# Optimization experiments

Measured on AMD Instinct MI355X. Metric: run time of the kernel, lower is better.

Reference implementation:

```python
import jax, jax.numpy as jnp
import numpy as np

B, S, E = 2048, 23, 768
RED, H, NUM_LABELS = 256, 8, 25
DH = RED // H
DELTA = 0.1
EPS_LN = 1e-5


def setup_inputs() -> dict:
    key = jax.random.key(0)
    ks = jax.random.split(key, 20)
    g = lambda k, shape, fan: jax.random.normal(k, shape, dtype=jnp.float32) * (1.0 / np.sqrt(fan))
    inp = {
        'cls_embeddings': jax.random.normal(ks[0], (B, S, E), dtype=jnp.float32),
        'existing_mask': jax.random.randint(ks[1], (B, S), 0, 2, dtype=jnp.int32),
        'missing_emb': g(ks[2], (S, E), E),
        'W1': g(ks[3], (E // 2, E), E), 'b1': jnp.zeros((E // 2,), jnp.float32),
        'W2': g(ks[4], (RED, E // 2), E // 2), 'b2': jnp.zeros((RED,), jnp.float32),
        'ln_g': jnp.ones((RED,), jnp.float32), 'ln_b': jnp.zeros((RED,), jnp.float32),
        'Wq': g(ks[5], (RED, RED), RED), 'bq': jnp.zeros((RED,), jnp.float32),
        'Wk': g(ks[6], (RED, RED), RED), 'bk': jnp.zeros((RED,), jnp.float32),
        'Wv': g(ks[7], (RED, RED), RED), 'bv': jnp.zeros((RED,), jnp.float32),
        'Wo': g(ks[8], (RED, RED), RED), 'bo': jnp.zeros((RED,), jnp.float32),
        'Wp': g(ks[9], (NUM_LABELS, RED), RED), 'bp': jnp.zeros((NUM_LABELS,), jnp.float32),
    }
    return inp


def _layer_norm(x, g, b):
    mu = jnp.mean(x, axis=-1, keepdims=True)
    var = jnp.mean(jnp.square(x - mu), axis=-1, keepdims=True)
    return (x - mu) * jax.lax.rsqrt(var + EPS_LN) * g + b


def _forward(cls_embeddings, existing_mask, missing_emb, W1, b1, W2, b2, ln_g, ln_b,
             Wq, bq, Wk, bk, Wv, bv, Wo, bo, Wp, bp):
    exist = existing_mask > 0                              # [B,S] bool
    # Gather: existing sections use BERT CLS, missing slots use learned embeddings
    sec = jnp.where(exist[..., None], cls_embeddings, missing_emb[None])  # [B,S,E]
    # SectionDimReducer (exact-erf GELU as in nn.GELU default)
    h = jax.nn.gelu(sec @ W1.T + b1, approximate=False)
    h = jax.nn.gelu(h @ W2.T + b2, approximate=False)
    red = _layer_norm(h, ln_g, ln_b)                       # [B,S,RED]
    # Tiny MHA: every slot queries the existing sections of its own EHR
    q = (red @ Wq.T + bq).reshape(B, S, H, DH)
    k = (red @ Wk.T + bk).reshape(B, S, H, DH)
    v = (red @ Wv.T + bv).reshape(B, S, H, DH)
    scores = jnp.einsum('bqhd,bkhd->bhqk', q, k) / np.sqrt(DH)
    scores = jnp.where(exist[:, None, None, :], scores, -1e9)
    attn = jax.nn.softmax(scores, axis=-1)                 # [B,H,S,S]
    ctx = jnp.einsum('bhqk,bkhd->bqhd', attn, v).reshape(B, S, RED)
    mha_out = ctx @ Wo.T + bo                              # [B,S,RED]
    # Scatter: only missing slots (of EHRs with >=1 existing section) are replaced
    any_exist = jnp.any(exist, axis=1)                     # [B]
    use_attn = (~exist) & any_exist[:, None]               # [B,S]
    updated = jnp.where(use_attn[..., None], mha_out, red)
    # margin-based orthogonality loss on section embeddings
    norm = updated / jnp.maximum(jnp.linalg.norm(updated, axis=-1, keepdims=True), 1e-8)
    gram = jnp.einsum('bid,bjd->bij', norm, norm)          # [B,S,S]
    off = 1.0 - jnp.eye(S, dtype=updated.dtype)
    loss_orth = jnp.sum(jax.nn.relu(jnp.abs(gram) - DELTA) * off) / (B * S * (S - 1))
    logits = updated.mean(axis=1) @ Wp.T + bp              # [B,NUM_LABELS]
    return loss_orth, logits


def reference(cls_embeddings, existing_mask, missing_emb, W1, b1, W2, b2, ln_g, ln_b,
              Wq, bq, Wk, bk, Wv, bv, Wo, bo, Wp, bp):
    return _forward(cls_embeddings, existing_mask, missing_emb, W1, b1, W2, b2, ln_g, ln_b,
                    Wq, bq, Wk, bk, Wv, bv, Wo, bo, Wp, bp)
```

## Files before the change

### kernel.cpp

```cpp
#include <hip/hip_runtime.h>

typedef unsigned short u16;
typedef unsigned int u32;
typedef __attribute__((ext_vector_type(8))) short short8;
typedef __attribute__((ext_vector_type(4))) float f32x4;

struct __align__(8) us4 { u16 x, y, z, w; };

__device__ __forceinline__ float bf1(u16 v){ return __uint_as_float(((u32)v) << 16); }
__device__ __forceinline__ float bflo(u32 u){ return __uint_as_float(u << 16); }
__device__ __forceinline__ float bfhi(u32 u){ return __uint_as_float(u & 0xFFFF0000u); }
__device__ __forceinline__ u16 fbf(float f){
    u32 u = __float_as_uint(f);
    return (u16)((u + 0x7FFFu + ((u >> 16) & 1u)) >> 16);
}
__device__ __forceinline__ float gelu_exact(float x){
    return 0.5f * x * (1.0f + erff(x * 0.70710678118654752f));
}
__device__ __forceinline__ void unp8(uint4 u, float* f){
    f[0]=bflo(u.x); f[1]=bfhi(u.x); f[2]=bflo(u.y); f[3]=bfhi(u.y);
    f[4]=bflo(u.z); f[5]=bfhi(u.z); f[6]=bflo(u.w); f[7]=bfhi(u.w);
}
__device__ __forceinline__ uint4 pack8(float4 a, float4 b){
    uint4 u;
    u.x = (u32)fbf(a.x) | ((u32)fbf(a.y) << 16);
    u.y = (u32)fbf(a.z) | ((u32)fbf(a.w) << 16);
    u.z = (u32)fbf(b.x) | ((u32)fbf(b.y) << 16);
    u.w = (u32)fbf(b.z) | ((u32)fbf(b.w) << 16);
    return u;
}

#define MFMA16(a, b, c) __builtin_amdgcn_mfma_f32_16x16x32_bf16(a, b, c, 0, 0, 0)
#define QSTR 264


__global__ __launch_bounds__(256) void wconv(
    const float* __restrict__ W1, const float* __restrict__ W2,
    const float* __restrict__ Wq, const float* __restrict__ Wk,
    const float* __restrict__ Wv, const float* __restrict__ Wo,
    const float* __restrict__ Wp, u16* __restrict__ dst)
{
    const int i = blockIdx.x * 256 + threadIdx.x;
    const float* s; int o;
    if      (i < 294912) { s = W1; o = i; }
    else if (i < 393216) { s = W2; o = i - 294912; }
    else if (i < 458752) { s = Wq; o = i - 393216; }
    else if (i < 524288) { s = Wk; o = i - 458752; }
    else if (i < 589824) { s = Wv; o = i - 524288; }
    else if (i < 655360) { s = Wo; o = i - 589824; }
    else                 { s = Wp; o = i - 655360; }
    dst[i] = fbf(s[o]);
}

__global__ __launch_bounds__(256) void gemm1_kernel(
    const float* __restrict__ cls, const int* __restrict__ mask,
    const float* __restrict__ missing, const u16* __restrict__ W,
    const float* __restrict__ bias, u16* __restrict__ C)
{
    const int K = 768, M = 384;
    __shared__ u16 As[128 * 40];
    __shared__ u16 Bs[128 * 40];
    const int tid = threadIdx.x;
    const int w = tid >> 6, lane = tid & 63;
    const int nBase = blockIdx.y * 128, mBase = blockIdx.x * 128;
    const int wr = w >> 1, wc = w & 1;
    const int r0 = tid >> 2;
    const int co = (tid & 3) * 8;
    const int frow = lane & 15, quad = lane >> 4;

    const int rowA0 = nBase + r0, rowA1 = nBase + r0 + 64;
    const float* ap0 = (mask[rowA0] > 0) ? cls + (size_t)rowA0 * 768
                                         : missing + (size_t)(rowA0 % 23) * 768;
    const float* ap1 = (mask[rowA1] > 0) ? cls + (size_t)rowA1 * 768
                                         : missing + (size_t)(rowA1 % 23) * 768;
    const u16* bp0 = W + (size_t)(mBase + r0) * K;
    const u16* bp1 = W + (size_t)(mBase + r0 + 64) * K;

    f32x4 acc[4][4];
#pragma unroll
    for (int mt = 0; mt < 4; ++mt)
#pragma unroll
        for (int nt = 0; nt < 4; ++nt) acc[mt][nt] = f32x4{0.f, 0.f, 0.f, 0.f};

    float4 a0a = *(const float4*)(ap0 + co), a0b = *(const float4*)(ap0 + co + 4);
    float4 a1a = *(const float4*)(ap1 + co), a1b = *(const float4*)(ap1 + co + 4);
    uint4 pb0 = *(const uint4*)(bp0 + co), pb1 = *(const uint4*)(bp1 + co);

    for (int k0 = 0; k0 < K; k0 += 32) {
        __syncthreads();
        *(uint4*)(As + r0 * 40 + co) = pack8(a0a, a0b);
        *(uint4*)(As + (r0 + 64) * 40 + co) = pack8(a1a, a1b);
        *(uint4*)(Bs + r0 * 40 + co) = pb0;
        *(uint4*)(Bs + (r0 + 64) * 40 + co) = pb1;
        __syncthreads();
        if (k0 + 32 < K) {
            const int kn = k0 + 32 + co;
            a0a = *(const float4*)(ap0 + kn); a0b = *(const float4*)(ap0 + kn + 4);
            a1a = *(const float4*)(ap1 + kn); a1b = *(const float4*)(ap1 + kn + 4);
            pb0 = *(const uint4*)(bp0 + kn);  pb1 = *(const uint4*)(bp1 + kn);
        }
        short8 af[4], bfv[4];
#pragma unroll
        for (int mt = 0; mt < 4; ++mt)
            af[mt] = *(const short8*)(As + (wr * 64 + mt * 16 + frow) * 40 + quad * 8);
#pragma unroll
        for (int nt = 0; nt < 4; ++nt)
            bfv[nt] = *(const short8*)(Bs + (wc * 64 + nt * 16 + frow) * 40 + quad * 8);
#pragma unroll
        for (int mt = 0; mt < 4; ++mt)
#pragma unroll
            for (int nt = 0; nt < 4; ++nt)
                acc[mt][nt] = MFMA16(af[mt], bfv[nt], acc[mt][nt]);
    }

#pragma unroll
    for (int nt = 0; nt < 4; ++nt) {
        const int col = mBase + wc * 64 + nt * 16 + frow;
        const float bv = bias[col];
#pragma unroll
        for (int mt = 0; mt < 4; ++mt)
#pragma unroll
            for (int reg = 0; reg < 4; ++reg) {
                const int row = nBase + wr * 64 + mt * 16 + quad * 4 + reg;
                C[(size_t)row * M + col] = fbf(gelu_exact(acc[mt][nt][reg] + bv));
            }
    }
}

__global__ __launch_bounds__(256) void gemm_bt(
    const u16* __restrict__ A, const u16* __restrict__ W,
    const float* __restrict__ bias, u16* __restrict__ C, int K, int M)
{
    __shared__ u16 As[128 * 40];
    __shared__ u16 Bs[128 * 40];
    const int tid = threadIdx.x;
    const int w = tid >> 6, lane = tid & 63;
    const int nBase = blockIdx.y * 128, mBase = blockIdx.x * 128;
    const int wr = w >> 1, wc = w & 1;
    const int r0 = tid >> 2;
    const int co = (tid & 3) * 8;
    const int frow = lane & 15, quad = lane >> 4;

    f32x4 acc[4][4];
#pragma unroll
    for (int mt = 0; mt < 4; ++mt)
#pragma unroll
        for (int nt = 0; nt < 4; ++nt) acc[mt][nt] = f32x4{0.f, 0.f, 0.f, 0.f};

    uint4 pa0 = *(const uint4*)(A + (size_t)(nBase + r0) * K + co);
    uint4 pa1 = *(const uint4*)(A + (size_t)(nBase + r0 + 64) * K + co);
    uint4 pb0 = *(const uint4*)(W + (size_t)(mBase + r0) * K + co);
    uint4 pb1 = *(const uint4*)(W + (size_t)(mBase + r0 + 64) * K + co);

    for (int k0 = 0; k0 < K; k0 += 32) {
        __syncthreads();
        *(uint4*)(As + r0 * 40 + co) = pa0;
        *(uint4*)(As + (r0 + 64) * 40 + co) = pa1;
        *(uint4*)(Bs + r0 * 40 + co) = pb0;
        *(uint4*)(Bs + (r0 + 64) * 40 + co) = pb1;
        __syncthreads();
        if (k0 + 32 < K) {
            const int kn = k0 + 32 + co;
            pa0 = *(const uint4*)(A + (size_t)(nBase + r0) * K + kn);
            pa1 = *(const uint4*)(A + (size_t)(nBase + r0 + 64) * K + kn);
            pb0 = *(const uint4*)(W + (size_t)(mBase + r0) * K + kn);
            pb1 = *(const uint4*)(W + (size_t)(mBase + r0 + 64) * K + kn);
        }
        short8 af[4], bfv[4];
#pragma unroll
        for (int mt = 0; mt < 4; ++mt)
            af[mt] = *(const short8*)(As + (wr * 64 + mt * 16 + frow) * 40 + quad * 8);
#pragma unroll
        for (int nt = 0; nt < 4; ++nt)
            bfv[nt] = *(const short8*)(Bs + (wc * 64 + nt * 16 + frow) * 40 + quad * 8);
#pragma unroll
        for (int mt = 0; mt < 4; ++mt)
#pragma unroll
            for (int nt = 0; nt < 4; ++nt)
                acc[mt][nt] = MFMA16(af[mt], bfv[nt], acc[mt][nt]);
    }

#pragma unroll
    for (int nt = 0; nt < 4; ++nt) {
        const int col = mBase + wc * 64 + nt * 16 + frow;
        const float bv = bias[col];
#pragma unroll
        for (int mt = 0; mt < 4; ++mt)
#pragma unroll
            for (int reg = 0; reg < 4; ++reg) {
                const int row = nBase + wr * 64 + mt * 16 + quad * 4 + reg;
                C[(size_t)row * M + col] = fbf(gelu_exact(acc[mt][nt][reg] + bv));
            }
    }
}

__device__ __forceinline__ void ln1_reg(
    const float* x, const float4& g0, const float4& g1,
    const float4& b0, const float4& b1, u16* rp)
{
    float s = x[0] + x[1] + x[2] + x[3] + x[4] + x[5] + x[6] + x[7];
    s += __shfl_xor(s, 1); s += __shfl_xor(s, 2); s += __shfl_xor(s, 4);
    s += __shfl_xor(s, 8); s += __shfl_xor(s, 16);
    const float mu = s * (1.f / 256.f);
    float v = 0.f;
#pragma unroll
    for (int e = 0; e < 8; ++e) { const float d = x[e] - mu; v += d * d; }
    v += __shfl_xor(v, 1); v += __shfl_xor(v, 2); v += __shfl_xor(v, 4);
    v += __shfl_xor(v, 8); v += __shfl_xor(v, 16);
    const float rs = rsqrtf(v * (1.f / 256.f) + 1e-5f);
    float4 ya, yb;
    ya.x = (x[0]-mu)*rs*g0.x + b0.x;
    ya.y = (x[1]-mu)*rs*g0.y + b0.y;
    ya.z = (x[2]-mu)*rs*g0.z + b0.z;
    ya.w = (x[3]-mu)*rs*g0.w + b0.w;
    yb.x = (x[4]-mu)*rs*g1.x + b1.x;
    yb.y = (x[5]-mu)*rs*g1.y + b1.y;
    yb.z = (x[6]-mu)*rs*g1.z + b1.z;
    yb.w = (x[7]-mu)*rs*g1.w + b1.w;
    *(uint4*)rp = pack8(ya, yb);
}

__device__ __forceinline__ void ln3_reg_store(
    uint4 rg0, uint4 rg1, uint4 rg2, bool has2,
    const float* __restrict__ lng, const float* __restrict__ lnb,
    u16* dstBase, int s0, int c0o)
{
    const float4 g0 = *(const float4*)(lng + c0o);
    const float4 g1 = *(const float4*)(lng + c0o + 4);
    const float4 b0 = *(const float4*)(lnb + c0o);
    const float4 b1 = *(const float4*)(lnb + c0o + 4);
    float x[8];
    unp8(rg0, x); ln1_reg(x, g0, g1, b0, b1, dstBase + s0 * QSTR + c0o);
    unp8(rg1, x); ln1_reg(x, g0, g1, b0, b1, dstBase + (s0 + 8) * QSTR + c0o);
    if (has2) { unp8(rg2, x); ln1_reg(x, g0, g1, b0, b1, dstBase + (s0 + 16) * QSTR + c0o); }
}

#define KLOOP_PF(WPTR, SRC, ACC)                                                  \
    {                                                                             \
        short8 nb0 = *(const short8*)(WPTR);                                      \
        short8 nb1 = *(const short8*)((WPTR) + 16 * 256);                         \
        short8 nb2 = *(const short8*)((WPTR) + 32 * 256);                         \
        short8 nb3 = *(const short8*)((WPTR) + 48 * 256);                         \
        for (int k0 = 0; k0 < 256; k0 += 32) {                                    \
            short8 a0 = *(const short8*)((SRC) + r0c * QSTR + k0 + quad * 8);     \
            short8 a1 = *(const short8*)((SRC) + r1c * QSTR + k0 + quad * 8);     \
            short8 c0 = nb0, c1 = nb1, c2 = nb2, c3 = nb3;                        \
            if (k0 + 32 < 256) {                                                  \
                nb0 = *(const short8*)((WPTR) + (k0 + 32));                       \
                nb1 = *(const short8*)((WPTR) + 16 * 256 + (k0 + 32));            \
                nb2 = *(const short8*)((WPTR) + 32 * 256 + (k0 + 32));            \
                nb3 = *(const short8*)((WPTR) + 48 * 256 + (k0 + 32));            \
            }                                                                     \
            ACC[0][0] = MFMA16(a0, c0, ACC[0][0]); ACC[1][0] = MFMA16(a1, c0, ACC[1][0]); \
            ACC[0][1] = MFMA16(a0, c1, ACC[0][1]); ACC[1][1] = MFMA16(a1, c1, ACC[1][1]); \
            ACC[0][2] = MFMA16(a0, c2, ACC[0][2]); ACC[1][2] = MFMA16(a1, c2, ACC[1][2]); \
            ACC[0][3] = MFMA16(a0, c3, ACC[0][3]); ACC[1][3] = MFMA16(a1, c3, ACC[1][3]); \
        }                                                                         \
    }

__global__ __launch_bounds__(256, 3) void attn_tail_kernel(
    const u16* __restrict__ redb, const int* __restrict__ mask,
    const u16* __restrict__ Wqkvb,
    const float* __restrict__ bq, const float* __restrict__ bk,
    const float* __restrict__ bv, const u16* __restrict__ Wob,
    const float* __restrict__ bo, const float* __restrict__ lng,
    const float* __restrict__ lnb, const u16* __restrict__ Wpb,
    const float* __restrict__ bp, float* __restrict__ out,
    float* __restrict__ lossAcc)
{
    __shared__ __align__(16) unsigned char SM[40960];
    u16* s_rq = (u16*)SM;
    u16* s_k  = (u16*)(SM + 12144);
    u16* s_vT = (u16*)(SM + 24288);
    int* sEx   = (int*)(SM + 40672);
    int* sMiss = (int*)(SM + 40764);
    float* sDiag = (float*)(SM + 24288);
    float* sInv  = (float*)(SM + 24384);
    float* sPool = (float*)(SM + 24480);

    const int b = blockIdx.x, t = threadIdx.x;
    const int w = t >> 6, lane = t & 63;
    const int frow = lane & 15, quad = lane >> 4;
    const int r0c = frow;
    const int r1c = (16 + frow > 22) ? 22 : 16 + frow;
    const f32x4 z4 = f32x4{0.f, 0.f, 0.f, 0.f};

    {
        const int myEx = (t < 23) ? mask[b * 23 + t] : 0;
        if (t < 23) sEx[t] = myEx;
        if (t < 64) {
            const unsigned long long ball = __ballot((t < 23) && (myEx > 0));
            if (t < 23) sMiss[t] = (ball != 0ull && myEx <= 0) ? 1 : 0;
        }
    }
    for (int i = t; i < 1024; i += 256) ((uint4*)s_vT)[i] = make_uint4(0u, 0u, 0u, 0u);

    {
        const u16* src = redb + (size_t)(b * 23) * 256;
        const int s0 = t >> 5, c0o = (t & 31) * 8;
        uint4 rg0 = *(const uint4*)(src + s0 * 256 + c0o);
        uint4 rg1 = *(const uint4*)(src + (s0 + 8) * 256 + c0o);
        uint4 rg2 = make_uint4(0u, 0u, 0u, 0u);
        const bool has2 = t < 224;
        if (has2) rg2 = *(const uint4*)(src + (s0 + 16) * 256 + c0o);
        ln3_reg_store(rg0, rg1, rg2, has2, lng, lnb, s_rq, s0, c0o);
    }
    __syncthreads();

    const int cmb = w * 64 + frow;
    {
        f32x4 ka[2][4];
#pragma unroll
        for (int mt = 0; mt < 2; ++mt)
#pragma unroll
            for (int nt = 0; nt < 4; ++nt) ka[mt][nt] = z4;
        const u16* wp = Wqkvb + (size_t)(256 + cmb) * 256 + quad * 8;
        const float bb[4] = {bk[cmb], bk[cmb + 16], bk[cmb + 32], bk[cmb + 48]};
        KLOOP_PF(wp, s_rq, ka)
#pragma unroll
        for (int nt = 0; nt < 4; ++nt) {
            const int cm = cmb + nt * 16;
#pragma unroll
            for (int mt = 0; mt < 2; ++mt)
#pragma unroll
                for (int reg = 0; reg < 4; ++reg) {
                    const int s = mt * 16 + quad * 4 + reg;
                    if (s < 23) s_k[s * QSTR + cm] = fbf(ka[mt][nt][reg] + bb[nt]);
                }
        }
    }
    {
        f32x4 va[2][4];
#pragma unroll
        for (int mt = 0; mt < 2; ++mt)
#pragma unroll
            for (int nt = 0; nt < 4; ++nt) va[mt][nt] = z4;
        const u16* wp = Wqkvb + (size_t)(512 + cmb) * 256 + quad * 8;
        const float bb[4] = {bv[cmb], bv[cmb + 16], bv[cmb + 32], bv[cmb + 48]};
        KLOOP_PF(wp, s_rq, va)
#pragma unroll
        for (int nt = 0; nt < 4; ++nt) {
            const int cm = cmb + nt * 16;
#pragma unroll
            for (int mt = 0; mt < 2; ++mt)
#pragma unroll
                for (int reg = 0; reg < 4; ++reg) {
                    const int s = mt * 16 + quad * 4 + reg;
                    if (s < 23) s_vT[cm * 32 + s] = fbf(va[mt][nt][reg] + bb[nt]);
                }
        }
    }
    {
        f32x4 qa[2][4];
#pragma unroll
        for (int mt = 0; mt < 2; ++mt)
#pragma unroll
            for (int nt = 0; nt < 4; ++nt) qa[mt][nt] = z4;
        const u16* wp = Wqkvb + (size_t)cmb * 256 + quad * 8;
        const float bb[4] = {bq[cmb], bq[cmb + 16], bq[cmb + 32], bq[cmb + 48]};
        KLOOP_PF(wp, s_rq, qa)
        __syncthreads();
#pragma unroll
        for (int nt = 0; nt < 4; ++nt) {
            const int cm = cmb + nt * 16;
#pragma unroll
            for (int mt = 0; mt < 2; ++mt)
#pragma unroll
                for (int reg = 0; reg < 4; ++reg) {
                    const int s = mt * 16 + quad * 4 + reg;
                    if (s < 23) s_rq[s * QSTR + cm] = fbf(qa[mt][nt][reg] + bb[nt]);
                }
        }
    }

    {
        const float scl = 0.17677669529663687f;
        const float m0 = (sEx[frow] > 0) ? 0.f : -1e9f;
        const float m1 = (16 + frow < 23 && sEx[16 + frow] > 0) ? 0.f : -1e9f;
#pragma unroll
        for (int hh2 = 0; hh2 < 2; ++hh2) {
            const int hb = w * 64 + hh2 * 32;
            short8 aq0 = *(const short8*)(s_rq + r0c * QSTR + hb + quad * 8);
            short8 aq1 = *(const short8*)(s_rq + r1c * QSTR + hb + quad * 8);
            short8 bk0 = *(const short8*)(s_k + r0c * QSTR + hb + quad * 8);
            short8 bk1 = *(const short8*)(s_k + r1c * QSTR + hb + quad * 8);
            f32x4 s00 = MFMA16(aq0, bk0, z4);
            f32x4 s01 = MFMA16(aq0, bk1, z4);
            f32x4 s10 = MFMA16(aq1, bk0, z4);
            f32x4 s11 = MFMA16(aq1, bk1, z4);
#pragma unroll
            for (int mt = 0; mt < 2; ++mt) {
                f32x4& c0 = mt ? s10 : s00;
                f32x4& c1 = mt ? s11 : s01;
#pragma unroll
                for (int reg = 0; reg < 4; ++reg) {
                    float v0 = c0[reg] * scl + m0;
                    float v1 = c1[reg] * scl + m1;
                    float mx = fmaxf(v0, v1);
#pragma unroll
                    for (int m = 8; m; m >>= 1) mx = fmaxf(mx, __shfl_xor(mx, m));
                    float p0 = __expf(v0 - mx), p1 = __expf(v1 - mx);
                    float sm = p0 + p1;
#pragma unroll
                    for (int m = 8; m; m >>= 1) sm += __shfl_xor(sm, m);
                    const float inv = 1.f / sm;
                    c0[reg] = p0 * inv;
                    c1[reg] = p1 * inv;
                }
            }
#pragma unroll
            for (int reg = 0; reg < 4; ++reg) {
                const int q0r = quad * 4 + reg;
                s_k[q0r * QSTR + hb + frow]      = fbf(s00[reg]);
                s_k[q0r * QSTR + hb + 16 + frow] = fbf(s01[reg]);
                const int q1r = 16 + quad * 4 + reg;
                if (q1r < 23) {
                    s_k[q1r * QSTR + hb + frow]      = fbf(s10[reg]);
                    s_k[q1r * QSTR + hb + 16 + frow] = fbf(s11[reg]);
                }
            }
            short8 pa0 = *(const short8*)(s_k + r0c * QSTR + hb + quad * 8);
            short8 pa1 = *(const short8*)(s_k + r1c * QSTR + hb + quad * 8);
            short8 bv0 = *(const short8*)(s_vT + (hb + frow) * 32 + quad * 8);
            short8 bv1 = *(const short8*)(s_vT + (hb + 16 + frow) * 32 + quad * 8);
            f32x4 c00 = MFMA16(pa0, bv0, z4);
            f32x4 c01 = MFMA16(pa0, bv1, z4);
            f32x4 c10 = MFMA16(pa1, bv0, z4);
            f32x4 c11 = MFMA16(pa1, bv1, z4);
#pragma unroll
            for (int reg = 0; reg < 4; ++reg) {
                const int q0r = quad * 4 + reg;
                s_rq[q0r * QSTR + hb + frow]      = fbf(c00[reg]);
                s_rq[q0r * QSTR + hb + 16 + frow] = fbf(c01[reg]);
                const int q1r = 16 + quad * 4 + reg;
                if (q1r < 23) {
                    s_rq[q1r * QSTR + hb + frow]      = fbf(c10[reg]);
                    s_rq[q1r * QSTR + hb + 16 + frow] = fbf(c11[reg]);
                }
            }
        }
    }
    __syncthreads();

    {
        f32x4 wacc[2][4];
#pragma unroll
        for (int mt = 0; mt < 2; ++mt)
#pragma unroll
            for (int nt = 0; nt < 4; ++nt) wacc[mt][nt] = z4;
        const u16* wp = Wob + (size_t)cmb * 256 + quad * 8;
        const float ob[4] = {bo[cmb], bo[cmb + 16], bo[cmb + 32], bo[cmb + 48]};
        KLOOP_PF(wp, s_rq, wacc)
        {
            const u16* src = redb + (size_t)(b * 23) * 256;
            const int s0 = t >> 5, c0o = (t & 31) * 8;
            uint4 rg0 = *(const uint4*)(src + s0 * 256 + c0o);
            uint4 rg1 = *(const uint4*)(src + (s0 + 8) * 256 + c0o);
            uint4 rg2 = make_uint4(0u, 0u, 0u, 0u);
            const bool has2 = t < 224;
            if (has2) rg2 = *(const uint4*)(src + (s0 + 16) * 256 + c0o);
            ln3_reg_store(rg0, rg1, rg2, has2, lng, lnb, s_k, s0, c0o);
        }
        __syncthreads();
#pragma unroll
        for (int nt = 0; nt < 4; ++nt) {
            const int col = cmb + nt * 16;
#pragma unroll
            for (int mt = 0; mt < 2; ++mt)
#pragma unroll
                for (int reg = 0; reg < 4; ++reg) {
                    const int s = mt * 16 + quad * 4 + reg;
                    if (s < 23 && sMiss[s])
                        s_k[s * QSTR + col] = fbf(wacc[mt][nt][reg] + ob[nt]);
                }
        }
    }
    __syncthreads();

    f32x4 g00 = z4, g01 = z4, g10 = z4, g11 = z4;
    if (w == 0) {
        short8 ga0 = *(const short8*)(s_k + r0c * QSTR + quad * 8);
        short8 ga1 = *(const short8*)(s_k + r1c * QSTR + quad * 8);
        for (int k0 = 0; k0 < 256; k0 += 32) {
            short8 a0 = ga0, a1 = ga1;
            if (k0 + 32 < 256) {
                ga0 = *(const short8*)(s_k + r0c * QSTR + k0 + 32 + quad * 8);
                ga1 = *(const short8*)(s_k + r1c * QSTR + k0 + 32 + quad * 8);
            }
            g00 = MFMA16(a0, a0, g00);
            g01 = MFMA16(a0, a1, g01);
            g10 = MFMA16(a1, a0, g10);
            g11 = MFMA16(a1, a1, g11);
        }
#pragma unroll
        for (int reg = 0; reg < 4; ++reg) {
            if (frow == quad * 4 + reg) {
                sDiag[frow] = g00[reg];
                if (16 + frow < 23) sDiag[16 + frow] = g11[reg];
            }
        }
    } else {
        for (int c = t - 64; c < 256; c += 192) {
            float pv = 0.f;
#pragma unroll
            for (int s = 0; s < 23; ++s) pv += bf1(s_k[s * QSTR + c]);
            sPool[c] = pv * (1.f / 23.f);
        }
    }
    __syncthreads();
    if (t < 23) sInv[t] = 1.f / fmaxf(sqrtf(sDiag[t]), 1e-8f);
    __syncthreads();

    if (w == 0) {
        float contrib = 0.f;
        const float ic0 = sInv[frow];
        const float ic1 = (16 + frow < 23) ? sInv[16 + frow] : 0.f;
        const bool c1ok = (16 + frow < 23);
#pragma unroll
        for (int reg = 0; reg < 4; ++reg) {
            const int rA = quad * 4 + reg;
            const float irA = sInv[rA];
            if (rA != frow) {
                const float cc = fabsf(g00[reg] * irA * ic0) - 0.1f;
                if (cc > 0.f) contrib += cc;
            }
            if (c1ok) {
                const float cc = fabsf(g01[reg] * irA * ic1) - 0.1f;
                if (cc > 0.f) contrib += cc;
            }
            const int rB = 16 + quad * 4 + reg;
            if (rB < 23) {
                const float irB = sInv[rB];
                {
                    const float cc = fabsf(g10[reg] * irB * ic0) - 0.1f;
                    if (cc > 0.f) contrib += cc;
                }
                if (c1ok && rB != 16 + frow) {
                    const float cc = fabsf(g11[reg] * irB * ic1) - 0.1f;
                    if (cc > 0.f) contrib += cc;
                }
            }
        }
#pragma unroll
        for (int m = 32; m; m >>= 1) contrib += __shfl_xor(contrib, m);
        if (lane == 0) atomicAdd(lossAcc, contrib);
    } else {
        const int li = t - 64;
        {
            const int L = li >> 3, chunk = li & 7;
            float a = 0.f;
#pragma unroll
            for (int q4 = 0; q4 < 4; ++q4) {
                const int c8 = chunk * 4 + q4;
                float wf[8]; unp8(*(const uint4*)(Wpb + (size_t)L * 256 + c8 * 8), wf);
                const float4 p0 = *(const float4*)(sPool + c8 * 8);
                const float4 p1 = *(const float4*)(sPool + c8 * 8 + 4);
                a += wf[0] * p0.x + wf[1] * p0.y + wf[2] * p0.z + wf[3] * p0.w
                   + wf[4] * p1.x + wf[5] * p1.y + wf[6] * p1.z + wf[7] * p1.w;
            }
            a += __shfl_xor(a, 1); a += __shfl_xor(a, 2); a += __shfl_xor(a, 4);
            if (chunk == 0) out[1 + b * 25 + L] = a + bp[L];
        }
        if (li < 8) {
            float a = 0.f;
#pragma unroll
            for (int q4 = 0; q4 < 4; ++q4) {
                const int c8 = li * 4 + q4;
                float wf[8]; unp8(*(const uint4*)(Wpb + (size_t)24 * 256 + c8 * 8), wf);
                const float4 p0 = *(const float4*)(sPool + c8 * 8);
                const float4 p1 = *(const float4*)(sPool + c8 * 8 + 4);
                a += wf[0] * p0.x + wf[1] * p0.y + wf[2] * p0.z + wf[3] * p0.w
                   + wf[4] * p1.x + wf[5] * p1.y + wf[6] * p1.z + wf[7] * p1.w;
            }
            a += __shfl_xor(a, 1); a += __shfl_xor(a, 2); a += __shfl_xor(a, 4);
            if (li == 0) out[1 + b * 25 + 24] = a + bp[24];
        }
    }
}

__global__ void loss_finalize(const float* __restrict__ lossAcc, float* __restrict__ out)
{
    out[0] = lossAcc[0] * (1.f / 1036288.f);
}

extern "C" void kernel_launch(void* const* d_in, const int* in_sizes, int n_in,
                              void* d_out, int out_size, void* d_ws, size_t ws_size,
                              hipStream_t stream)
{
    const float* cls     = (const float*)d_in[0];
    const int*   mask    = (const int*)d_in[1];
    const float* missing = (const float*)d_in[2];
    const float* W1 = (const float*)d_in[3];  const float* b1 = (const float*)d_in[4];
    const float* W2 = (const float*)d_in[5];  const float* b2 = (const float*)d_in[6];
    const float* lng = (const float*)d_in[7]; const float* lnb = (const float*)d_in[8];
    const float* Wq = (const float*)d_in[9];  const float* bq = (const float*)d_in[10];
    const float* Wk = (const float*)d_in[11]; const float* bk = (const float*)d_in[12];
    const float* Wv = (const float*)d_in[13]; const float* bv = (const float*)d_in[14];
    const float* Wo = (const float*)d_in[15]; const float* bo = (const float*)d_in[16];
    const float* Wp = (const float*)d_in[17]; const float* bp = (const float*)d_in[18];
    float* out = (float*)d_out;

    char* ws = (char*)d_ws;
    u16* h1b  = (u16*)ws;
    u16* redb = (u16*)(ws + 36175872);
    u16* Wb   = (u16*)(ws + 60293120);
    u16* W1b   = Wb;
    u16* W2b   = Wb + 294912;
    u16* Wqkvb = Wb + 393216;
    u16* Wob   = Wb + 589824;
    u16* Wpb   = Wb + 655360;
    float* lossAcc = (float*)(ws + 61616640);

    hipMemsetAsync(lossAcc, 0, sizeof(float), stream);

    wconv<<<2585, 256, 0, stream>>>(W1, W2, Wq, Wk, Wv, Wo, Wp, Wb);
    gemm1_kernel<<<dim3(3, 368), 256, 0, stream>>>(cls, mask, missing, W1b, b1, h1b);
    gemm_bt<<<dim3(2, 368), 256, 0, stream>>>(h1b, W2b, b2, redb, 384, 256);
    attn_tail_kernel<<<2048, 256, 0, stream>>>(redb, mask, Wqkvb, bq, bk, bv,
                                               Wob, bo, lng, lnb, Wpb, bp,
                                               out, lossAcc);
    loss_finalize<<<1, 1, 0, stream>>>(lossAcc, out);
}
```

Measured before the change: 529.7 us.

## Compact existing rows and compute missing-slot reductions once per slot

Adds a scan kernel that compacts rows whose mask is set into a dense list after the 23 unique missing-embedding rows. The two reducer GEMMs then run only over the compacted rows and exit early for tiles beyond the count. The attention tail gathers reduced rows through an index map. This removes redundant GEMM work on duplicated missing-embedding rows, roughly halving the rows processed, at the cost of an extra kernel, atomics, gathered loads and nondeterministic row order.

```diff
diff --git a/kernel.cpp b/kernel.cpp
--- a/kernel.cpp
+++ b/kernel.cpp
@@ -32,6 +32,7 @@
 
 #define MFMA16(a, b, c) __builtin_amdgcn_mfma_f32_16x16x32_bf16(a, b, c, 0, 0, 0)
 #define QSTR 264
+#define CAPROWS 46208
 
 
 __global__ __launch_bounds__(256) void wconv(
@@ -52,27 +53,45 @@
     dst[i] = fbf(s[o]);
 }
 
+__global__ __launch_bounds__(256) void scan_kernel(
+    const int* __restrict__ mask, int* __restrict__ idx,
+    int* __restrict__ rowsrc, int* __restrict__ cnt)
+{
+    const int i = blockIdx.x * 256 + threadIdx.x;
+    if (blockIdx.x == 0 && threadIdx.x < 23)
+        rowsrc[threadIdx.x] = -(threadIdx.x + 1);
+    if (mask[i] > 0) {
+        const int slot = 23 + atomicAdd(cnt, 1);
+        idx[i] = slot;
+        rowsrc[slot] = i;
+    }
+}
+
 __global__ __launch_bounds__(256) void gemm1_kernel(
-    const float* __restrict__ cls, const int* __restrict__ mask,
-    const float* __restrict__ missing, const u16* __restrict__ W,
-    const float* __restrict__ bias, u16* __restrict__ C)
+    const float* __restrict__ cls, const int* __restrict__ rowsrc,
+    const int* __restrict__ cnt, const float* __restrict__ missing,
+    const u16* __restrict__ W, const float* __restrict__ bias,
+    u16* __restrict__ C)
 {
     const int K = 768, M = 384;
+    const int nBase = blockIdx.y * 128;
+    if (nBase >= *cnt + 23) return;
     __shared__ u16 As[128 * 40];
     __shared__ u16 Bs[128 * 40];
     const int tid = threadIdx.x;
     const int w = tid >> 6, lane = tid & 63;
-    const int nBase = blockIdx.y * 128, mBase = blockIdx.x * 128;
+    const int mBase = blockIdx.x * 128;
     const int wr = w >> 1, wc = w & 1;
     const int r0 = tid >> 2;
     const int co = (tid & 3) * 8;
     const int frow = lane & 15, quad = lane >> 4;
 
-    const int rowA0 = nBase + r0, rowA1 = nBase + r0 + 64;
-    const float* ap0 = (mask[rowA0] > 0) ? cls + (size_t)rowA0 * 768
-                                         : missing + (size_t)(rowA0 % 23) * 768;
-    const float* ap1 = (mask[rowA1] > 0) ? cls + (size_t)rowA1 * 768
-                                         : missing + (size_t)(rowA1 % 23) * 768;
+    const int rs0 = rowsrc[nBase + r0];
+    const int rs1 = rowsrc[nBase + r0 + 64];
+    const float* ap0 = (rs0 >= 0) ? cls + (size_t)rs0 * 768
+                                  : missing + (size_t)(-rs0 - 1) * 768;
+    const float* ap1 = (rs1 >= 0) ? cls + (size_t)rs1 * 768
+                                  : missing + (size_t)(-rs1 - 1) * 768;
     const u16* bp0 = W + (size_t)(mBase + r0) * K;
     const u16* bp1 = W + (size_t)(mBase + r0 + 64) * K;
 
@@ -129,13 +148,16 @@
 
 __global__ __launch_bounds__(256) void gemm_bt(
     const u16* __restrict__ A, const u16* __restrict__ W,
-    const float* __restrict__ bias, u16* __restrict__ C, int K, int M)
-{
+    const float* __restrict__ bias, u16* __restrict__ C, int K, int M,
+    const int* __restrict__ cnt)
+{
+    const int nBase = blockIdx.y * 128;
+    if (nBase >= *cnt + 23) return;
     __shared__ u16 As[128 * 40];
     __shared__ u16 Bs[128 * 40];
     const int tid = threadIdx.x;
     const int w = tid >> 6, lane = tid & 63;
-    const int nBase = blockIdx.y * 128, mBase = blockIdx.x * 128;
+    const int mBase = blockIdx.x * 128;
     const int wr = w >> 1, wc = w & 1;
     const int r0 = tid >> 2;
     const int co = (tid & 3) * 8;
@@ -260,6 +282,7 @@
 
 __global__ __launch_bounds__(256, 3) void attn_tail_kernel(
     const u16* __restrict__ redb, const int* __restrict__ mask,
+    const int* __restrict__ idxArr,
     const u16* __restrict__ Wqkvb,
     const float* __restrict__ bq, const float* __restrict__ bk,
     const float* __restrict__ bv, const u16* __restrict__ Wob,
@@ -274,6 +297,7 @@
     u16* s_vT = (u16*)(SM + 24288);
     int* sEx   = (int*)(SM + 40672);
     int* sMiss = (int*)(SM + 40764);
+    int* sCrow = (int*)(SM + 40856);
     float* sDiag = (float*)(SM + 24288);
     float* sInv  = (float*)(SM + 24384);
     float* sPool = (float*)(SM + 24480);
@@ -287,22 +311,25 @@
 
     {
         const int myEx = (t < 23) ? mask[b * 23 + t] : 0;
-        if (t < 23) sEx[t] = myEx;
+        if (t < 23) {
+            sEx[t] = myEx;
+            sCrow[t] = (myEx > 0) ? idxArr[b * 23 + t] : t;
+        }
         if (t < 64) {
             const unsigned long long ball = __ballot((t < 23) && (myEx > 0));
             if (t < 23) sMiss[t] = (ball != 0ull && myEx <= 0) ? 1 : 0;
         }
     }
     for (int i = t; i < 1024; i += 256) ((uint4*)s_vT)[i] = make_uint4(0u, 0u, 0u, 0u);
+    __syncthreads();
 
     {
-        const u16* src = redb + (size_t)(b * 23) * 256;
         const int s0 = t >> 5, c0o = (t & 31) * 8;
-        uint4 rg0 = *(const uint4*)(src + s0 * 256 + c0o);
-        uint4 rg1 = *(const uint4*)(src + (s0 + 8) * 256 + c0o);
+        uint4 rg0 = *(const uint4*)(redb + (size_t)sCrow[s0] * 256 + c0o);
+        uint4 rg1 = *(const uint4*)(redb + (size_t)sCrow[s0 + 8] * 256 + c0o);
         uint4 rg2 = make_uint4(0u, 0u, 0u, 0u);
         const bool has2 = t < 224;
-        if (has2) rg2 = *(const uint4*)(src + (s0 + 16) * 256 + c0o);
+        if (has2) rg2 = *(const uint4*)(redb + (size_t)sCrow[s0 + 16] * 256 + c0o);
         ln3_reg_store(rg0, rg1, rg2, has2, lng, lnb, s_rq, s0, c0o);
     }
     __syncthreads();
@@ -452,13 +479,12 @@
         const float ob[4] = {bo[cmb], bo[cmb + 16], bo[cmb + 32], bo[cmb + 48]};
         KLOOP_PF(wp, s_rq, wacc)
         {
-            const u16* src = redb + (size_t)(b * 23) * 256;
             const int s0 = t >> 5, c0o = (t & 31) * 8;
-            uint4 rg0 = *(const uint4*)(src + s0 * 256 + c0o);
-            uint4 rg1 = *(const uint4*)(src + (s0 + 8) * 256 + c0o);
+            uint4 rg0 = *(const uint4*)(redb + (size_t)sCrow[s0] * 256 + c0o);
+            uint4 rg1 = *(const uint4*)(redb + (size_t)sCrow[s0 + 8] * 256 + c0o);
             uint4 rg2 = make_uint4(0u, 0u, 0u, 0u);
             const bool has2 = t < 224;
-            if (has2) rg2 = *(const uint4*)(src + (s0 + 16) * 256 + c0o);
+            if (has2) rg2 = *(const uint4*)(redb + (size_t)sCrow[s0 + 16] * 256 + c0o);
             ln3_reg_store(rg0, rg1, rg2, has2, lng, lnb, s_k, s0, c0o);
         }
         __syncthreads();
@@ -602,21 +628,28 @@
 
     char* ws = (char*)d_ws;
     u16* h1b  = (u16*)ws;
-    u16* redb = (u16*)(ws + 36175872);
-    u16* Wb   = (u16*)(ws + 60293120);
+    u16* redb = (u16*)(ws + 35487744);
+    u16* Wb   = (u16*)(ws + 59146240);
     u16* W1b   = Wb;
     u16* W2b   = Wb + 294912;
     u16* Wqkvb = Wb + 393216;
     u16* Wob   = Wb + 589824;
     u16* Wpb   = Wb + 655360;
-    float* lossAcc = (float*)(ws + 61616640);
+    int* idx    = (int*)(ws + 60469760);
+    int* rowsrc = (int*)(ws + 60658176);
+    int* cnt    = (int*)(ws + 60843008);
+    float* lossAcc = (float*)(ws + 60843012);
 
     hipMemsetAsync(lossAcc, 0, sizeof(float), stream);
+    hipMemsetAsync(cnt, 0, sizeof(int), stream);
+    hipMemsetAsync(rowsrc, 0, CAPROWS * sizeof(int), stream);
 
     wconv<<<2585, 256, 0, stream>>>(W1, W2, Wq, Wk, Wv, Wo, Wp, Wb);
-    gemm1_kernel<<<dim3(3, 368), 256, 0, stream>>>(cls, mask, missing, W1b, b1, h1b);
-    gemm_bt<<<dim3(2, 368), 256, 0, stream>>>(h1b, W2b, b2, redb, 384, 256);
-    attn_tail_kernel<<<2048, 256, 0, stream>>>(redb, mask, Wqkvb, bq, bk, bv,
+    scan_kernel<<<184, 256, 0, stream>>>(mask, idx, rowsrc, cnt);
+    gemm1_kernel<<<dim3(3, 361), 256, 0, stream>>>(cls, rowsrc, cnt, missing,
+                                                   W1b, b1, h1b);
+    gemm_bt<<<dim3(2, 361), 256, 0, stream>>>(h1b, W2b, b2, redb, 384, 256, cnt);
+    attn_tail_kernel<<<2048, 256, 0, stream>>>(redb, mask, idx, Wqkvb, bq, bk, bv,
                                                Wob, bo, lng, lnb, Wpb, bp,
                                                out, lossAcc);
     loss_finalize<<<1, 1, 0, stream>>>(lossAcc, out);
```

After: 507.5 us. 4.2% less time.
